# Optimization experiments

Hardware: AMD Instinct MI355X
Metric: run time of the kernel (lower is better)

Reference implementation:

```python
import jax, jax.numpy as jnp
import numpy as np

D_MODEL = 512
LR = 0.01
CLIP = 0.5
B, T = 8, 4096


def setup_inputs() -> dict:
    key = jax.random.key(0)
    k1, k2, k3 = jax.random.split(key, 3)
    x = jax.random.normal(k1, (B, T, D_MODEL), dtype=jnp.float32)
    W_current = jnp.zeros((D_MODEL, D_MODEL), dtype=jnp.float32)
    W_base = jax.random.normal(k2, (D_MODEL, D_MODEL), dtype=jnp.float32) * 0.02
    gate_w = jax.random.normal(k3, (D_MODEL, D_MODEL), dtype=jnp.float32) * (1.0 / np.sqrt(D_MODEL))
    gate_b = jnp.zeros((D_MODEL,), dtype=jnp.float32)
    return {"x": x, "W_current": W_current, "W_base": W_base, "gate_w": gate_w, "gate_b": gate_b}


def reference(x, W_current, W_base, gate_w, gate_b):
    # x: [B, T, D]; W_current, W_base, gate_w: [D, D]; gate_b: [D]
    def step(W_c, x_t):  # x_t: [B, D]
        W = W_base + W_c
        mem_read = x_t @ W.T                       # [B, D]
        gate = jax.nn.sigmoid(x_t @ gate_w.T + gate_b)
        out_t = gate * mem_read
        # fast-weight update (torch.no_grad -> stop_gradient)
        surprise_avg = jax.lax.stop_gradient((x_t - mem_read).mean(axis=0))
        x_avg = jax.lax.stop_gradient(x_t.mean(axis=0))
        dW = jnp.outer(surprise_avg, x_avg)        # [D, D]
        n = jnp.linalg.norm(dW)
        dW = dW * jnp.where(n > CLIP, CLIP / n, 1.0)
        W_new = W_c + LR * dW
        return W_new, out_t

    xs = jnp.swapaxes(x, 0, 1)                     # [T, B, D]
    W_final, outs = jax.lax.scan(step, W_current, xs)
    out = jnp.swapaxes(outs, 0, 1)                 # [B, T, D]
    return out, W_final
```

## Files before the change

kernel.cpp:

```cpp
#include <hip/hip_runtime.h>
#include <math.h>

#define BB 8
#define TT 4096
#define DD 512
constexpr float LRF = 0.01f;

#define OFF_A  0
#define OFF_CU 2097152
#define OFF_G  4194304
#define OFF_P  5242880
#define OFF_BV 5373952
#define OFF_W  5406720
#define OFF_WS 5668864
#define OFF_S  9863168

__global__ void tm_mean(const float* __restrict__ x, float* __restrict__ a) {
    int idx = blockIdx.x * 256 + threadIdx.x;
    float s = 0.f;
#pragma unroll
    for (int b = 0; b < BB; ++b) s += x[b * (TT * DD) + idx];
    a[idx] = s * 0.125f;
}

__global__ void tm_init(const float* __restrict__ wb, const float* __restrict__ wc,
                        float* __restrict__ W, float* __restrict__ Wsnap) {
    int idx = blockIdx.x * 256 + threadIdx.x;
    float v = wb[idx] + wc[idx];
    W[idx] = v;
    Wsnap[idx] = v;
}

__global__ __launch_bounds__(256) void tm_gram(const float* __restrict__ a, float* __restrict__ G) {
    __shared__ float sl[64 * 65];
    __shared__ float tl[64 * 65];
    int bid = blockIdx.x;
    int p = bid >> 4, ts = (bid >> 2) & 3, tt = bid & 3;
    int tid = threadIdx.x;
    int c0 = (tid & 15) * 4, r0 = (tid >> 4) * 4;
    float acc[4][4] = {};
    for (int kt = 0; kt < 8; ++kt) {
        if (kt) __syncthreads();
        for (int l = tid; l < 64 * 16; l += 256) {
            int r = l >> 4, c4 = (l & 15) * 4;
            float4 v = *(const float4*)&a[(p * 256 + ts * 64 + r) * DD + kt * 64 + c4];
            sl[r * 65 + c4] = v.x; sl[r * 65 + c4 + 1] = v.y;
            sl[r * 65 + c4 + 2] = v.z; sl[r * 65 + c4 + 3] = v.w;
            float4 u = *(const float4*)&a[(p * 256 + tt * 64 + r) * DD + kt * 64 + c4];
            tl[r * 65 + c4] = u.x; tl[r * 65 + c4 + 1] = u.y;
            tl[r * 65 + c4 + 2] = u.z; tl[r * 65 + c4 + 3] = u.w;
        }
        __syncthreads();
        for (int kk = 0; kk < 64; ++kk) {
            float as[4], at[4];
#pragma unroll
            for (int q = 0; q < 4; ++q) { as[q] = sl[(r0 + q) * 65 + kk]; at[q] = tl[(c0 + q) * 65 + kk]; }
#pragma unroll
            for (int q = 0; q < 4; ++q)
#pragma unroll
                for (int w2 = 0; w2 < 4; ++w2) acc[q][w2] += as[q] * at[w2];
        }
    }
#pragma unroll
    for (int q = 0; q < 4; ++q) {
        float4 v = make_float4(acc[q][0], acc[q][1], acc[q][2], acc[q][3]);
        *(float4*)&G[p * 65536 + (ts * 64 + r0 + q) * 256 + tt * 64 + c0] = v;
    }
}

__global__ __launch_bounds__(256) void tm_P(const float* __restrict__ a, const float* __restrict__ W,
                                            float* __restrict__ P, int p) {
    __shared__ float al[64 * 65];
    __shared__ float wl[64 * 65];
    int bid = blockIdx.x;
    int bt = bid & 3, bi = bid >> 2;
    int tid = threadIdx.x;
    int c0 = (tid & 15) * 4, r0 = (tid >> 4) * 4;
    float acc[4][4] = {};
    for (int kt = 0; kt < 8; ++kt) {
        if (kt) __syncthreads();
        for (int l = tid; l < 64 * 16; l += 256) {
            int r = l >> 4, c4 = (l & 15) * 4;
            float4 v = *(const float4*)&a[(p * 256 + bt * 64 + r) * DD + kt * 64 + c4];
            al[r * 65 + c4] = v.x; al[r * 65 + c4 + 1] = v.y;
            al[r * 65 + c4 + 2] = v.z; al[r * 65 + c4 + 3] = v.w;
            float4 u = *(const float4*)&W[(bi * 64 + r) * DD + kt * 64 + c4];
            wl[r * 65 + c4] = u.x; wl[r * 65 + c4 + 1] = u.y;
            wl[r * 65 + c4 + 2] = u.z; wl[r * 65 + c4 + 3] = u.w;
        }
        __syncthreads();
        for (int kk = 0; kk < 64; ++kk) {
            float af[4], bf[4];
#pragma unroll
            for (int q = 0; q < 4; ++q) { af[q] = al[(r0 + q) * 65 + kk]; bf[q] = wl[(c0 + q) * 65 + kk]; }
#pragma unroll
            for (int q = 0; q < 4; ++q)
#pragma unroll
                for (int w2 = 0; w2 < 4; ++w2) acc[q][w2] += af[q] * bf[w2];
        }
    }
#pragma unroll
    for (int q = 0; q < 4; ++q) {
        float4 av = *(const float4*)&a[(p * 256 + bt * 64 + r0 + q) * DD + bi * 64 + c0];
        float4 v = make_float4(av.x - acc[q][0], av.y - acc[q][1],
                               av.z - acc[q][2], av.w - acc[q][3]);
        *(float4*)&P[(bt * 64 + r0 + q) * DD + bi * 64 + c0] = v;
    }
}

__global__ __launch_bounds__(256) void tm_corr(const float* __restrict__ P, const float* __restrict__ G,
                                               const float* __restrict__ CU, float* __restrict__ bv,
                                               int p, int j) {
    __shared__ float gsl[64 * 65];
    __shared__ float cul[64 * 65];
    int bd = blockIdx.x;
    int tid = threadIdx.x;
    int c0 = (tid & 15) * 4, r0 = (tid >> 4) * 4;
    const float* Gp = G + p * 65536;
    float acc[4][4] = {};
    for (int kb = 0; kb < j * 64; kb += 64) {
        if (kb) __syncthreads();
        for (int l = tid; l < 64 * 16; l += 256) {
            int r = l >> 4, c4 = (l & 15) * 4;
            float4 v = *(const float4*)&Gp[(kb + r) * 256 + j * 64 + c4];
            gsl[r * 65 + c4] = v.x; gsl[r * 65 + c4 + 1] = v.y;
            gsl[r * 65 + c4 + 2] = v.z; gsl[r * 65 + c4 + 3] = v.w;
            float4 u = *(const float4*)&CU[(p * 256 + kb + r) * DD + bd * 64 + c4];
            cul[r * 65 + c4] = u.x; cul[r * 65 + c4 + 1] = u.y;
            cul[r * 65 + c4 + 2] = u.z; cul[r * 65 + c4 + 3] = u.w;
        }
        __syncthreads();
        for (int kk = 0; kk < 64; ++kk) {
            float gf[4], cf[4];
#pragma unroll
            for (int q = 0; q < 4; ++q) { gf[q] = gsl[kk * 65 + r0 + q]; cf[q] = cul[kk * 65 + c0 + q]; }
#pragma unroll
            for (int q = 0; q < 4; ++q)
#pragma unroll
                for (int w2 = 0; w2 < 4; ++w2) acc[q][w2] += gf[q] * cf[w2];
        }
    }
#pragma unroll
    for (int q = 0; q < 4; ++q) {
        float4 pv = *(const float4*)&P[(j * 64 + r0 + q) * DD + bd * 64 + c0];
        float4 v = make_float4(pv.x - LRF * acc[q][0], pv.y - LRF * acc[q][1],
                               pv.z - LRF * acc[q][2], pv.w - LRF * acc[q][3]);
        *(float4*)&bv[(r0 + q) * DD + bd * 64 + c0] = v;
    }
}

__global__ __launch_bounds__(256) void tm_scan(const float* __restrict__ bv, const float* __restrict__ G,
                                               float* __restrict__ cu, int kchunk) {
    __shared__ float gl[64 * 64];
    __shared__ float part[2][4];
    int tid = threadIdx.x;
    int wid = tid >> 6, lane = tid & 63;
    int p = kchunk >> 2, j = kchunk & 3;
    const float* Gp = G + p * 65536;
    for (int l = tid; l < 64 * 16; l += 256) {
        int r = l >> 4, c4 = (l & 15) * 4;
        float4 v = *(const float4*)&Gp[(j * 64 + r) * 256 + j * 64 + c4];
        *(float4*)&gl[r * 64 + c4] = v;
    }
    float acc0[64], acc1[64];
#pragma unroll
    for (int t = 0; t < 64; ++t) {
        acc0[t] = bv[t * DD + tid];
        acc1[t] = bv[t * DD + tid + 256];
    }
    __syncthreads();
    float* cup = cu + (p * 256 + j * 64) * DD;
#pragma unroll
    for (int s = 0; s < 64; ++s) {
        float u0 = acc0[s], u1 = acc1[s];
        float v = u0 * u0 + u1 * u1;
#pragma unroll
        for (int off = 32; off > 0; off >>= 1) v += __shfl_xor(v, off, 64);
        if (lane == 0) part[s & 1][wid] = v;
        __syncthreads();
        float n2u = part[s & 1][0] + part[s & 1][1] + part[s & 1][2] + part[s & 1][3];
        float n2 = n2u * gl[s * 64 + s];
        float cs = (n2 > 0.25f) ? 0.5f * rsqrtf(n2) : 1.0f;
        cup[s * DD + tid] = cs * u0;
        cup[s * DD + tid + 256] = cs * u1;
        float w0 = (LRF * cs) * u0, w1 = (LRF * cs) * u1;
        int t0 = s + 1;
#pragma unroll
        for (; t0 < 64 && (t0 & 3); ++t0) {
            float g = gl[s * 64 + t0];
            acc0[t0] -= g * w0; acc1[t0] -= g * w1;
        }
#pragma unroll
        for (; t0 < 64; t0 += 4) {
            float4 g4 = *(const float4*)&gl[s * 64 + t0];
            acc0[t0]     -= g4.x * w0; acc1[t0]     -= g4.x * w1;
            acc0[t0 + 1] -= g4.y * w0; acc1[t0 + 1] -= g4.y * w1;
            acc0[t0 + 2] -= g4.z * w0; acc1[t0 + 2] -= g4.z * w1;
            acc0[t0 + 3] -= g4.w * w0; acc1[t0 + 3] -= g4.w * w1;
        }
    }
}

__global__ void tm_wupd(const float* __restrict__ a, const float* __restrict__ cu,
                        float* __restrict__ W, float* __restrict__ Wsnap,
                        const float* __restrict__ wb, float* __restrict__ outW,
                        int p, int snap_p, int is_final) {
    int idx = blockIdx.x * 256 + threadIdx.x;
    int i = idx >> 9, jj = idx & 511;
    const float* cb = cu + p * 256 * DD + i;
    const float* ab = a + p * 256 * DD + jj;
    float s = 0.f;
#pragma unroll 8
    for (int r = 0; r < 256; ++r) s += cb[r * DD] * ab[r * DD];
    float w = W[idx] + LRF * s;
    W[idx] = w;
    if (snap_p >= 0) Wsnap[snap_p * DD * DD + idx] = w;
    if (is_final) outW[idx] = w - wb[idx];
}


__global__ __launch_bounds__(256) void tm_mem(const float* __restrict__ x, const float* __restrict__ Wsnap,
                                              float* __restrict__ out) {
    __shared__ float al[64 * 65];
    __shared__ float bl[64 * 65];
    int bid = blockIdx.x;
    int p = bid >> 8, rem = bid & 255, rt = rem >> 3, it = rem & 7;
    int tid = threadIdx.x;
    int c0 = (tid & 15) * 4, r0 = (tid >> 4) * 4;
    const float* Wp = Wsnap + p * DD * DD;
    float acc[4][4] = {};
    for (int kt = 0; kt < 8; ++kt) {
        if (kt) __syncthreads();
        for (int l = tid; l < 64 * 16; l += 256) {
            int r = l >> 4, c4 = (l & 15) * 4;
            int rloc = rt * 64 + r;
            int grow = ((rloc >> 8) * TT) + p * 256 + (rloc & 255);
            float4 v = *(const float4*)&x[grow * DD + kt * 64 + c4];
            al[r * 65 + c4] = v.x; al[r * 65 + c4 + 1] = v.y;
            al[r * 65 + c4 + 2] = v.z; al[r * 65 + c4 + 3] = v.w;
            float4 u = *(const float4*)&Wp[(it * 64 + r) * DD + kt * 64 + c4];
            bl[r * 65 + c4] = u.x; bl[r * 65 + c4 + 1] = u.y;
            bl[r * 65 + c4 + 2] = u.z; bl[r * 65 + c4 + 3] = u.w;
        }
        __syncthreads();
        for (int kk = 0; kk < 64; ++kk) {
            float af[4], bf[4];
#pragma unroll
            for (int q = 0; q < 4; ++q) { af[q] = al[(r0 + q) * 65 + kk]; bf[q] = bl[(c0 + q) * 65 + kk]; }
#pragma unroll
            for (int q = 0; q < 4; ++q)
#pragma unroll
                for (int w2 = 0; w2 < 4; ++w2) acc[q][w2] += af[q] * bf[w2];
        }
    }
#pragma unroll
    for (int q = 0; q < 4; ++q) {
        int rloc = rt * 64 + r0 + q;
        int grow = ((rloc >> 8) * TT) + p * 256 + (rloc & 255);
        float4 v = make_float4(acc[q][0], acc[q][1], acc[q][2], acc[q][3]);
        *(float4*)&out[grow * DD + it * 64 + c0] = v;
    }
}

__global__ __launch_bounds__(256) void tm_score(const float* __restrict__ x, const float* __restrict__ a,
                                                float* __restrict__ S) {
    __shared__ float al[64 * 65];
    __shared__ float bl[64 * 65];
    int bid = blockIdx.x;
    int st = bid & 3, rt = (bid >> 2) & 31, p = bid >> 7;
    int tid = threadIdx.x;
    int c0 = (tid & 15) * 4, r0 = (tid >> 4) * 4;
    float acc[4][4] = {};
    for (int kt = 0; kt < 8; ++kt) {
        if (kt) __syncthreads();
        for (int l = tid; l < 64 * 16; l += 256) {
            int r = l >> 4, c4 = (l & 15) * 4;
            int rloc = rt * 64 + r;
            int grow = ((rloc >> 8) * TT) + p * 256 + (rloc & 255);
            float4 v = *(const float4*)&x[grow * DD + kt * 64 + c4];
            al[r * 65 + c4] = v.x; al[r * 65 + c4 + 1] = v.y;
            al[r * 65 + c4 + 2] = v.z; al[r * 65 + c4 + 3] = v.w;
            float4 u = *(const float4*)&a[(p * 256 + st * 64 + r) * DD + kt * 64 + c4];
            bl[r * 65 + c4] = u.x; bl[r * 65 + c4 + 1] = u.y;
            bl[r * 65 + c4 + 2] = u.z; bl[r * 65 + c4 + 3] = u.w;
        }
        __syncthreads();
        for (int kk = 0; kk < 64; ++kk) {
            float af[4], bf[4];
#pragma unroll
            for (int q = 0; q < 4; ++q) { af[q] = al[(r0 + q) * 65 + kk]; bf[q] = bl[(c0 + q) * 65 + kk]; }
#pragma unroll
            for (int q = 0; q < 4; ++q)
#pragma unroll
                for (int w2 = 0; w2 < 4; ++w2) acc[q][w2] += af[q] * bf[w2];
        }
    }
#pragma unroll
    for (int q = 0; q < 4; ++q) {
        int rloc = rt * 64 + r0 + q;
        float4 v = make_float4(acc[q][0], acc[q][1], acc[q][2], acc[q][3]);
        *(float4*)&S[(p * 2048 + rloc) * 256 + st * 64 + c0] = v;
    }
}

__global__ __launch_bounds__(256) void tm_apply(const float* __restrict__ S, const float* __restrict__ cu,
                                                float* __restrict__ out) {
    __shared__ float al[64 * 65];
    __shared__ float bl[64 * 65];
    int bid = blockIdx.x;
    int it = bid & 7, rt = (bid >> 3) & 31, p = bid >> 8;
    int tid = threadIdx.x;
    int c0 = (tid & 15) * 4, r0 = (tid >> 4) * 4;
    float acc[4][4] = {};
    for (int kt = 0; kt < 4; ++kt) {
        if (kt) __syncthreads();
        for (int l = tid; l < 64 * 16; l += 256) {
            int r = l >> 4, c4 = (l & 15) * 4;
            int rloc = rt * 64 + r;
            int tq = rloc & 255;
            float4 v = *(const float4*)&S[(p * 2048 + rloc) * 256 + kt * 64 + c4];
            int sb = kt * 64 + c4;
            al[r * 65 + c4]     = (sb + 0 < tq) ? v.x : 0.f;
            al[r * 65 + c4 + 1] = (sb + 1 < tq) ? v.y : 0.f;
            al[r * 65 + c4 + 2] = (sb + 2 < tq) ? v.z : 0.f;
            al[r * 65 + c4 + 3] = (sb + 3 < tq) ? v.w : 0.f;
            float4 u = *(const float4*)&cu[(p * 256 + kt * 64 + r) * DD + it * 64 + c4];
            bl[r * 65 + c4] = u.x; bl[r * 65 + c4 + 1] = u.y;
            bl[r * 65 + c4 + 2] = u.z; bl[r * 65 + c4 + 3] = u.w;
        }
        __syncthreads();
        for (int kk = 0; kk < 64; ++kk) {
            float af[4], bf[4];
#pragma unroll
            for (int q = 0; q < 4; ++q) { af[q] = al[(r0 + q) * 65 + kk]; bf[q] = bl[kk * 65 + c0 + q]; }
#pragma unroll
            for (int q = 0; q < 4; ++q)
#pragma unroll
                for (int w2 = 0; w2 < 4; ++w2) acc[q][w2] += af[q] * bf[w2];
        }
    }
#pragma unroll
    for (int q = 0; q < 4; ++q) {
        int rloc = rt * 64 + r0 + q;
        int grow = ((rloc >> 8) * TT) + p * 256 + (rloc & 255);
        float4 cur = *(float4*)&out[grow * DD + it * 64 + c0];
        cur.x += LRF * acc[q][0]; cur.y += LRF * acc[q][1];
        cur.z += LRF * acc[q][2]; cur.w += LRF * acc[q][3];
        *(float4*)&out[grow * DD + it * 64 + c0] = cur;
    }
}

__global__ __launch_bounds__(256) void tm_gate(const float* __restrict__ x, const float* __restrict__ gw,
                                               const float* __restrict__ gb, float* __restrict__ out) {
    __shared__ float al[64 * 65];
    __shared__ float bl[64 * 65];
    int bid = blockIdx.x;
    int it = bid & 7, rt = bid >> 3;
    int tid = threadIdx.x;
    int c0 = (tid & 15) * 4, r0 = (tid >> 4) * 4;
    float acc[4][4] = {};
    for (int kt = 0; kt < 8; ++kt) {
        if (kt) __syncthreads();
        for (int l = tid; l < 64 * 16; l += 256) {
            int r = l >> 4, c4 = (l & 15) * 4;
            int grow = rt * 64 + r;
            float4 v = *(const float4*)&x[grow * DD + kt * 64 + c4];
            al[r * 65 + c4] = v.x; al[r * 65 + c4 + 1] = v.y;
            al[r * 65 + c4 + 2] = v.z; al[r * 65 + c4 + 3] = v.w;
            float4 u = *(const float4*)&gw[(it * 64 + r) * DD + kt * 64 + c4];
            bl[r * 65 + c4] = u.x; bl[r * 65 + c4 + 1] = u.y;
            bl[r * 65 + c4 + 2] = u.z; bl[r * 65 + c4 + 3] = u.w;
        }
        __syncthreads();
        for (int kk = 0; kk < 64; ++kk) {
            float af[4], bf[4];
#pragma unroll
            for (int q = 0; q < 4; ++q) { af[q] = al[(r0 + q) * 65 + kk]; bf[q] = bl[(c0 + q) * 65 + kk]; }
#pragma unroll
            for (int q = 0; q < 4; ++q)
#pragma unroll
                for (int w2 = 0; w2 < 4; ++w2) acc[q][w2] += af[q] * bf[w2];
        }
    }
#pragma unroll
    for (int q = 0; q < 4; ++q) {
        int grow = rt * 64 + r0 + q;
        float4 cur = *(float4*)&out[grow * DD + it * 64 + c0];
        float z0 = acc[q][0] + gb[it * 64 + c0 + 0];
        float z1 = acc[q][1] + gb[it * 64 + c0 + 1];
        float z2 = acc[q][2] + gb[it * 64 + c0 + 2];
        float z3 = acc[q][3] + gb[it * 64 + c0 + 3];
        cur.x *= 1.f / (1.f + expf(-z0));
        cur.y *= 1.f / (1.f + expf(-z1));
        cur.z *= 1.f / (1.f + expf(-z2));
        cur.w *= 1.f / (1.f + expf(-z3));
        *(float4*)&out[grow * DD + it * 64 + c0] = cur;
    }
}

extern "C" void kernel_launch(void* const* d_in, const int* in_sizes, int n_in,
                              void* d_out, int out_size, void* d_ws, size_t ws_size,
                              hipStream_t stream) {
    const float* x   = (const float*)d_in[0];
    const float* Wc0 = (const float*)d_in[1];
    const float* Wb  = (const float*)d_in[2];
    const float* gw  = (const float*)d_in[3];
    const float* gb  = (const float*)d_in[4];
    float* out  = (float*)d_out;
    float* outW = out + BB * TT * DD;

    float* ws = (float*)d_ws;
    float* A  = ws + OFF_A;
    float* CU = ws + OFF_CU;
    float* G  = ws + OFF_G;
    float* P  = ws + OFF_P;
    float* BV = ws + OFF_BV;
    float* W  = ws + OFF_W;
    float* WS = ws + OFF_WS;
    float* S  = ws + OFF_S;

    tm_mean<<<(TT * DD) / 256, 256, 0, stream>>>(x, A);
    tm_init<<<(DD * DD) / 256, 256, 0, stream>>>(Wb, Wc0, W, WS);
    tm_gram<<<256, 256, 0, stream>>>(A, G);
    tm_P<<<32, 256, 0, stream>>>(A, W, P, 0);

    for (int p = 0; p < 16; ++p) {
        for (int j = 0; j < 4; ++j) {
            tm_corr<<<8, 256, 0, stream>>>(P, G, CU, BV, p, j);
            tm_scan<<<1, 256, 0, stream>>>(BV, G, CU, p * 4 + j);
        }
        if (p < 15) {
            tm_wupd<<<(DD * DD) / 256, 256, 0, stream>>>(A, CU, W, WS, Wb, outW, p, p + 1, 0);
            tm_P<<<32, 256, 0, stream>>>(A, W, P, p + 1);
        }
    }
    tm_wupd<<<(DD * DD) / 256, 256, 0, stream>>>(A, CU, W, WS, Wb, outW, 15, -1, 1);

    tm_mem<<<16 * 256, 256, 0, stream>>>(x, WS, out);
    tm_score<<<16 * 128, 256, 0, stream>>>(x, A, S);
    tm_apply<<<16 * 256, 256, 0, stream>>>(S, CU, out);
    tm_gate<<<512 * 8, 256, 0, stream>>>(x, gw, gb, out);
}
```

Baseline: 8.128 ms.

## Fuse chunk correction and scan into one kernel; transpose GEMM smem tiles

Replaces the per-subchunk tm_corr plus tm_scan pair (8 launches per period) with a single 512-thread tm_sc kernel. It scans all 256 steps of a period with each thread owning one column, applies the forward corrections to later subchunks in registers and global P, and reads the Gram matrix straight from global memory. Separately, the four GEMM kernels now store shared tiles transposed with a stride of 68, which allows float4 LDS reads and packed 2-wide FMAs. This cuts launch overhead on the serial critical path but leaves that path on one workgroup with heavy register use and uncached G reads. It also risks register spills from the b[64] and y[64] arrays.

```diff
diff --git a/kernel.cpp b/kernel.cpp
--- a/kernel.cpp
+++ b/kernel.cpp
@@ -5,6 +5,8 @@
 #define TT 4096
 #define DD 512
 constexpr float LRF = 0.01f;
+
+typedef float v2f __attribute__((ext_vector_type(2)));
 
 #define OFF_A  0
 #define OFF_CU 2097152
@@ -108,95 +110,72 @@
     }
 }
 
-__global__ __launch_bounds__(256) void tm_corr(const float* __restrict__ P, const float* __restrict__ G,
-                                               const float* __restrict__ CU, float* __restrict__ bv,
-                                               int p, int j) {
-    __shared__ float gsl[64 * 65];
-    __shared__ float cul[64 * 65];
-    int bd = blockIdx.x;
-    int tid = threadIdx.x;
-    int c0 = (tid & 15) * 4, r0 = (tid >> 4) * 4;
+__global__ __launch_bounds__(512) void tm_sc(const float* __restrict__ G,
+                                             float* __restrict__ P,
+                                             float* __restrict__ cu, int p) {
+    __shared__ float part[2][8];
+    int tid = threadIdx.x;
+    int wid = tid >> 6, lane = tid & 63;
     const float* Gp = G + p * 65536;
-    float acc[4][4] = {};
-    for (int kb = 0; kb < j * 64; kb += 64) {
-        if (kb) __syncthreads();
-        for (int l = tid; l < 64 * 16; l += 256) {
-            int r = l >> 4, c4 = (l & 15) * 4;
-            float4 v = *(const float4*)&Gp[(kb + r) * 256 + j * 64 + c4];
-            gsl[r * 65 + c4] = v.x; gsl[r * 65 + c4 + 1] = v.y;
-            gsl[r * 65 + c4 + 2] = v.z; gsl[r * 65 + c4 + 3] = v.w;
-            float4 u = *(const float4*)&CU[(p * 256 + kb + r) * DD + bd * 64 + c4];
-            cul[r * 65 + c4] = u.x; cul[r * 65 + c4 + 1] = u.y;
-            cul[r * 65 + c4 + 2] = u.z; cul[r * 65 + c4 + 3] = u.w;
-        }
-        __syncthreads();
-        for (int kk = 0; kk < 64; ++kk) {
-            float gf[4], cf[4];
-#pragma unroll
-            for (int q = 0; q < 4; ++q) { gf[q] = gsl[kk * 65 + r0 + q]; cf[q] = cul[kk * 65 + c0 + q]; }
-#pragma unroll
-            for (int q = 0; q < 4; ++q)
-#pragma unroll
-                for (int w2 = 0; w2 < 4; ++w2) acc[q][w2] += gf[q] * cf[w2];
-        }
-    }
-#pragma unroll
-    for (int q = 0; q < 4; ++q) {
-        float4 pv = *(const float4*)&P[(j * 64 + r0 + q) * DD + bd * 64 + c0];
-        float4 v = make_float4(pv.x - LRF * acc[q][0], pv.y - LRF * acc[q][1],
-                               pv.z - LRF * acc[q][2], pv.w - LRF * acc[q][3]);
-        *(float4*)&bv[(r0 + q) * DD + bd * 64 + c0] = v;
-    }
-}
-
-__global__ __launch_bounds__(256) void tm_scan(const float* __restrict__ bv, const float* __restrict__ G,
-                                               float* __restrict__ cu, int kchunk) {
-    __shared__ float gl[64 * 64];
-    __shared__ float part[2][4];
-    int tid = threadIdx.x;
-    int wid = tid >> 6, lane = tid & 63;
-    int p = kchunk >> 2, j = kchunk & 3;
-    const float* Gp = G + p * 65536;
-    for (int l = tid; l < 64 * 16; l += 256) {
-        int r = l >> 4, c4 = (l & 15) * 4;
-        float4 v = *(const float4*)&Gp[(j * 64 + r) * 256 + j * 64 + c4];
-        *(float4*)&gl[r * 64 + c4] = v;
-    }
-    float acc0[64], acc1[64];
-#pragma unroll
-    for (int t = 0; t < 64; ++t) {
-        acc0[t] = bv[t * DD + tid];
-        acc1[t] = bv[t * DD + tid + 256];
-    }
-    __syncthreads();
-    float* cup = cu + (p * 256 + j * 64) * DD;
-#pragma unroll
-    for (int s = 0; s < 64; ++s) {
-        float u0 = acc0[s], u1 = acc1[s];
-        float v = u0 * u0 + u1 * u1;
-#pragma unroll
-        for (int off = 32; off > 0; off >>= 1) v += __shfl_xor(v, off, 64);
-        if (lane == 0) part[s & 1][wid] = v;
-        __syncthreads();
-        float n2u = part[s & 1][0] + part[s & 1][1] + part[s & 1][2] + part[s & 1][3];
-        float n2 = n2u * gl[s * 64 + s];
-        float cs = (n2 > 0.25f) ? 0.5f * rsqrtf(n2) : 1.0f;
-        cup[s * DD + tid] = cs * u0;
-        cup[s * DD + tid + 256] = cs * u1;
-        float w0 = (LRF * cs) * u0, w1 = (LRF * cs) * u1;
-        int t0 = s + 1;
-#pragma unroll
-        for (; t0 < 64 && (t0 & 3); ++t0) {
-            float g = gl[s * 64 + t0];
-            acc0[t0] -= g * w0; acc1[t0] -= g * w1;
-        }
-#pragma unroll
-        for (; t0 < 64; t0 += 4) {
-            float4 g4 = *(const float4*)&gl[s * 64 + t0];
-            acc0[t0]     -= g4.x * w0; acc1[t0]     -= g4.x * w1;
-            acc0[t0 + 1] -= g4.y * w0; acc1[t0 + 1] -= g4.y * w1;
-            acc0[t0 + 2] -= g4.z * w0; acc1[t0 + 2] -= g4.z * w1;
-            acc0[t0 + 3] -= g4.w * w0; acc1[t0 + 3] -= g4.w * w1;
+    float* cup = cu + p * 256 * DD;
+    float b[64], y[64];
+#pragma unroll
+    for (int t = 0; t < 64; ++t) b[t] = P[t * DD + tid];
+
+    for (int j = 0; j < 4; ++j) {
+        const float* Gj = Gp + (j * 64) * 256;
+#pragma unroll
+        for (int s = 0; s < 64; ++s) {
+            float u = b[s];
+            float v = u * u;
+#pragma unroll
+            for (int off = 32; off > 0; off >>= 1) v += __shfl_xor(v, off, 64);
+            if (lane == 0) part[s & 1][wid] = v;
+            __syncthreads();
+            float n2u = 0.f;
+#pragma unroll
+            for (int w8 = 0; w8 < 8; ++w8) n2u += part[s & 1][w8];
+            float n2 = n2u * Gj[s * 256 + j * 64 + s];
+            float cs = (n2 > 0.25f) ? 0.5f * rsqrtf(n2) : 1.0f;
+            float yv = cs * u;
+            y[s] = yv;
+            float w = LRF * yv;
+            const float* gr = Gj + s * 256 + j * 64;
+#pragma unroll
+            for (int t = s + 1; t < 64; ++t) b[t] -= gr[t] * w;
+        }
+#pragma unroll
+        for (int s2 = 0; s2 < 64; ++s2) cup[(j * 64 + s2) * DD + tid] = y[s2];
+
+        if (j < 3) {
+#pragma unroll
+            for (int t = 0; t < 64; ++t) b[t] = P[((j + 1) * 64 + t) * DD + tid];
+#pragma unroll
+            for (int s = 0; s < 64; ++s) {
+                float w = LRF * y[s];
+                const float* gr = Gj + s * 256 + (j + 1) * 64;
+#pragma unroll
+                for (int t = 0; t < 64; ++t) b[t] -= gr[t] * w;
+            }
+            for (int jf = j + 2; jf < 4; ++jf) {
+                for (int tb = 0; tb < 4; ++tb) {
+                    float acc[16];
+#pragma unroll
+                    for (int t = 0; t < 16; ++t) acc[t] = 0.f;
+#pragma unroll
+                    for (int s = 0; s < 64; ++s) {
+                        const float* gr = Gj + s * 256 + jf * 64 + tb * 16;
+                        float ys = y[s];
+#pragma unroll
+                        for (int t = 0; t < 16; ++t) acc[t] += gr[t] * ys;
+                    }
+#pragma unroll
+                    for (int t = 0; t < 16; ++t) {
+                        int row = (jf * 64 + tb * 16 + t) * DD + tid;
+                        P[row] -= LRF * acc[t];
+                    }
+                }
+            }
         }
     }
 }
@@ -221,175 +200,170 @@
 
 __global__ __launch_bounds__(256) void tm_mem(const float* __restrict__ x, const float* __restrict__ Wsnap,
                                               float* __restrict__ out) {
-    __shared__ float al[64 * 65];
-    __shared__ float bl[64 * 65];
-    int bid = blockIdx.x;
-    int p = bid >> 8, rem = bid & 255, rt = rem >> 3, it = rem & 7;
-    int tid = threadIdx.x;
-    int c0 = (tid & 15) * 4, r0 = (tid >> 4) * 4;
-    const float* Wp = Wsnap + p * DD * DD;
-    float acc[4][4] = {};
+    __shared__ float al[64 * 68];
+    __shared__ float bl[64 * 68];
+    int bid = blockIdx.x;
+    int pp = bid >> 8, rem = bid & 255, rt = rem >> 3, it = rem & 7;
+    int tid = threadIdx.x;
+    int c0 = (tid & 15) * 4, r0 = (tid >> 4) * 4;
+    const float* Wp = Wsnap + pp * DD * DD;
+    v2f acc[4][2] = {};
     for (int kt = 0; kt < 8; ++kt) {
         if (kt) __syncthreads();
         for (int l = tid; l < 64 * 16; l += 256) {
             int r = l >> 4, c4 = (l & 15) * 4;
             int rloc = rt * 64 + r;
-            int grow = ((rloc >> 8) * TT) + p * 256 + (rloc & 255);
+            int grow = ((rloc >> 8) * TT) + pp * 256 + (rloc & 255);
             float4 v = *(const float4*)&x[grow * DD + kt * 64 + c4];
-            al[r * 65 + c4] = v.x; al[r * 65 + c4 + 1] = v.y;
-            al[r * 65 + c4 + 2] = v.z; al[r * 65 + c4 + 3] = v.w;
+            al[(c4 + 0) * 68 + r] = v.x; al[(c4 + 1) * 68 + r] = v.y;
+            al[(c4 + 2) * 68 + r] = v.z; al[(c4 + 3) * 68 + r] = v.w;
             float4 u = *(const float4*)&Wp[(it * 64 + r) * DD + kt * 64 + c4];
-            bl[r * 65 + c4] = u.x; bl[r * 65 + c4 + 1] = u.y;
-            bl[r * 65 + c4 + 2] = u.z; bl[r * 65 + c4 + 3] = u.w;
-        }
-        __syncthreads();
-        for (int kk = 0; kk < 64; ++kk) {
-            float af[4], bf[4];
-#pragma unroll
-            for (int q = 0; q < 4; ++q) { af[q] = al[(r0 + q) * 65 + kk]; bf[q] = bl[(c0 + q) * 65 + kk]; }
-#pragma unroll
-            for (int q = 0; q < 4; ++q)
-#pragma unroll
-                for (int w2 = 0; w2 < 4; ++w2) acc[q][w2] += af[q] * bf[w2];
+            bl[(c4 + 0) * 68 + r] = u.x; bl[(c4 + 1) * 68 + r] = u.y;
+            bl[(c4 + 2) * 68 + r] = u.z; bl[(c4 + 3) * 68 + r] = u.w;
+        }
+        __syncthreads();
+        for (int kk = 0; kk < 64; ++kk) {
+            float4 a4 = *(const float4*)&al[kk * 68 + r0];
+            float4 b4 = *(const float4*)&bl[kk * 68 + c0];
+            v2f blo = {b4.x, b4.y}, bhi = {b4.z, b4.w};
+            float af[4] = {a4.x, a4.y, a4.z, a4.w};
+#pragma unroll
+            for (int q = 0; q < 4; ++q) { acc[q][0] += af[q] * blo; acc[q][1] += af[q] * bhi; }
         }
     }
 #pragma unroll
     for (int q = 0; q < 4; ++q) {
         int rloc = rt * 64 + r0 + q;
-        int grow = ((rloc >> 8) * TT) + p * 256 + (rloc & 255);
-        float4 v = make_float4(acc[q][0], acc[q][1], acc[q][2], acc[q][3]);
+        int grow = ((rloc >> 8) * TT) + pp * 256 + (rloc & 255);
+        float4 v = make_float4(acc[q][0][0], acc[q][0][1], acc[q][1][0], acc[q][1][1]);
         *(float4*)&out[grow * DD + it * 64 + c0] = v;
     }
 }
 
 __global__ __launch_bounds__(256) void tm_score(const float* __restrict__ x, const float* __restrict__ a,
                                                 float* __restrict__ S) {
-    __shared__ float al[64 * 65];
-    __shared__ float bl[64 * 65];
-    int bid = blockIdx.x;
-    int st = bid & 3, rt = (bid >> 2) & 31, p = bid >> 7;
-    int tid = threadIdx.x;
-    int c0 = (tid & 15) * 4, r0 = (tid >> 4) * 4;
-    float acc[4][4] = {};
+    __shared__ float al[64 * 68];
+    __shared__ float bl[64 * 68];
+    int bid = blockIdx.x;
+    int st = bid & 3, rt = (bid >> 2) & 31, pp = bid >> 7;
+    int tid = threadIdx.x;
+    int c0 = (tid & 15) * 4, r0 = (tid >> 4) * 4;
+    v2f acc[4][2] = {};
     for (int kt = 0; kt < 8; ++kt) {
         if (kt) __syncthreads();
         for (int l = tid; l < 64 * 16; l += 256) {
             int r = l >> 4, c4 = (l & 15) * 4;
             int rloc = rt * 64 + r;
-            int grow = ((rloc >> 8) * TT) + p * 256 + (rloc & 255);
+            int grow = ((rloc >> 8) * TT) + pp * 256 + (rloc & 255);
             float4 v = *(const float4*)&x[grow * DD + kt * 64 + c4];
-            al[r * 65 + c4] = v.x; al[r * 65 + c4 + 1] = v.y;
-            al[r * 65 + c4 + 2] = v.z; al[r * 65 + c4 + 3] = v.w;
-            float4 u = *(const float4*)&a[(p * 256 + st * 64 + r) * DD + kt * 64 + c4];
-            bl[r * 65 + c4] = u.x; bl[r * 65 + c4 + 1] = u.y;
-            bl[r * 65 + c4 + 2] = u.z; bl[r * 65 + c4 + 3] = u.w;
-        }
-        __syncthreads();
-        for (int kk = 0; kk < 64; ++kk) {
-            float af[4], bf[4];
-#pragma unroll
-            for (int q = 0; q < 4; ++q) { af[q] = al[(r0 + q) * 65 + kk]; bf[q] = bl[(c0 + q) * 65 + kk]; }
-#pragma unroll
-            for (int q = 0; q < 4; ++q)
-#pragma unroll
-                for (int w2 = 0; w2 < 4; ++w2) acc[q][w2] += af[q] * bf[w2];
+            al[(c4 + 0) * 68 + r] = v.x; al[(c4 + 1) * 68 + r] = v.y;
+            al[(c4 + 2) * 68 + r] = v.z; al[(c4 + 3) * 68 + r] = v.w;
+            float4 u = *(const float4*)&a[(pp * 256 + st * 64 + r) * DD + kt * 64 + c4];
+            bl[(c4 + 0) * 68 + r] = u.x; bl[(c4 + 1) * 68 + r] = u.y;
+            bl[(c4 + 2) * 68 + r] = u.z; bl[(c4 + 3) * 68 + r] = u.w;
+        }
+        __syncthreads();
+        for (int kk = 0; kk < 64; ++kk) {
+            float4 a4 = *(const float4*)&al[kk * 68 + r0];
+            float4 b4 = *(const float4*)&bl[kk * 68 + c0];
+            v2f blo = {b4.x, b4.y}, bhi = {b4.z, b4.w};
+            float af[4] = {a4.x, a4.y, a4.z, a4.w};
+#pragma unroll
+            for (int q = 0; q < 4; ++q) { acc[q][0] += af[q] * blo; acc[q][1] += af[q] * bhi; }
         }
     }
 #pragma unroll
     for (int q = 0; q < 4; ++q) {
         int rloc = rt * 64 + r0 + q;
-        float4 v = make_float4(acc[q][0], acc[q][1], acc[q][2], acc[q][3]);
-        *(float4*)&S[(p * 2048 + rloc) * 256 + st * 64 + c0] = v;
+        float4 v = make_float4(acc[q][0][0], acc[q][0][1], acc[q][1][0], acc[q][1][1]);
+        *(float4*)&S[(pp * 2048 + rloc) * 256 + st * 64 + c0] = v;
     }
 }
 
 __global__ __launch_bounds__(256) void tm_apply(const float* __restrict__ S, const float* __restrict__ cu,
                                                 float* __restrict__ out) {
-    __shared__ float al[64 * 65];
-    __shared__ float bl[64 * 65];
-    int bid = blockIdx.x;
-    int it = bid & 7, rt = (bid >> 3) & 31, p = bid >> 8;
-    int tid = threadIdx.x;
-    int c0 = (tid & 15) * 4, r0 = (tid >> 4) * 4;
-    float acc[4][4] = {};
+    __shared__ float al[64 * 68];
+    __shared__ float bl[64 * 68];
+    int bid = blockIdx.x;
+    int it = bid & 7, rt = (bid >> 3) & 31, pp = bid >> 8;
+    int tid = threadIdx.x;
+    int c0 = (tid & 15) * 4, r0 = (tid >> 4) * 4;
+    v2f acc[4][2] = {};
     for (int kt = 0; kt < 4; ++kt) {
         if (kt) __syncthreads();
         for (int l = tid; l < 64 * 16; l += 256) {
             int r = l >> 4, c4 = (l & 15) * 4;
             int rloc = rt * 64 + r;
             int tq = rloc & 255;
-            float4 v = *(const float4*)&S[(p * 2048 + rloc) * 256 + kt * 64 + c4];
+            float4 v = *(const float4*)&S[(pp * 2048 + rloc) * 256 + kt * 64 + c4];
             int sb = kt * 64 + c4;
-            al[r * 65 + c4]     = (sb + 0 < tq) ? v.x : 0.f;
-            al[r * 65 + c4 + 1] = (sb + 1 < tq) ? v.y : 0.f;
-            al[r * 65 + c4 + 2] = (sb + 2 < tq) ? v.z : 0.f;
-            al[r * 65 + c4 + 3] = (sb + 3 < tq) ? v.w : 0.f;
-            float4 u = *(const float4*)&cu[(p * 256 + kt * 64 + r) * DD + it * 64 + c4];
-            bl[r * 65 + c4] = u.x; bl[r * 65 + c4 + 1] = u.y;
-            bl[r * 65 + c4 + 2] = u.z; bl[r * 65 + c4 + 3] = u.w;
-        }
-        __syncthreads();
-        for (int kk = 0; kk < 64; ++kk) {
-            float af[4], bf[4];
-#pragma unroll
-            for (int q = 0; q < 4; ++q) { af[q] = al[(r0 + q) * 65 + kk]; bf[q] = bl[kk * 65 + c0 + q]; }
-#pragma unroll
-            for (int q = 0; q < 4; ++q)
-#pragma unroll
-                for (int w2 = 0; w2 < 4; ++w2) acc[q][w2] += af[q] * bf[w2];
+            al[(c4 + 0) * 68 + r] = (sb + 0 < tq) ? v.x : 0.f;
+            al[(c4 + 1) * 68 + r] = (sb + 1 < tq) ? v.y : 0.f;
+            al[(c4 + 2) * 68 + r] = (sb + 2 < tq) ? v.z : 0.f;
+            al[(c4 + 3) * 68 + r] = (sb + 3 < tq) ? v.w : 0.f;
+            float4 u = *(const float4*)&cu[(pp * 256 + kt * 64 + r) * DD + it * 64 + c4];
+            *(float4*)&bl[r * 68 + c4] = u;
+        }
+        __syncthreads();
+        for (int kk = 0; kk < 64; ++kk) {
+            float4 a4 = *(const float4*)&al[kk * 68 + r0];
+            float4 b4 = *(const float4*)&bl[kk * 68 + c0];
+            v2f blo = {b4.x, b4.y}, bhi = {b4.z, b4.w};
+            float af[4] = {a4.x, a4.y, a4.z, a4.w};
+#pragma unroll
+            for (int q = 0; q < 4; ++q) { acc[q][0] += af[q] * blo; acc[q][1] += af[q] * bhi; }
         }
     }
 #pragma unroll
     for (int q = 0; q < 4; ++q) {
         int rloc = rt * 64 + r0 + q;
-        int grow = ((rloc >> 8) * TT) + p * 256 + (rloc & 255);
+        int grow = ((rloc >> 8) * TT) + pp * 256 + (rloc & 255);
         float4 cur = *(float4*)&out[grow * DD + it * 64 + c0];
-        cur.x += LRF * acc[q][0]; cur.y += LRF * acc[q][1];
-        cur.z += LRF * acc[q][2]; cur.w += LRF * acc[q][3];
+        cur.x += LRF * acc[q][0][0]; cur.y += LRF * acc[q][0][1];
+        cur.z += LRF * acc[q][1][0]; cur.w += LRF * acc[q][1][1];
         *(float4*)&out[grow * DD + it * 64 + c0] = cur;
     }
 }
 
 __global__ __launch_bounds__(256) void tm_gate(const float* __restrict__ x, const float* __restrict__ gw,
                                                const float* __restrict__ gb, float* __restrict__ out) {
-    __shared__ float al[64 * 65];
-    __shared__ float bl[64 * 65];
+    __shared__ float al[64 * 68];
+    __shared__ float bl[64 * 68];
     int bid = blockIdx.x;
     int it = bid & 7, rt = bid >> 3;
     int tid = threadIdx.x;
     int c0 = (tid & 15) * 4, r0 = (tid >> 4) * 4;
-    float acc[4][4] = {};
+    v2f acc[4][2] = {};
     for (int kt = 0; kt < 8; ++kt) {
         if (kt) __syncthreads();
         for (int l = tid; l < 64 * 16; l += 256) {
             int r = l >> 4, c4 = (l & 15) * 4;
             int grow = rt * 64 + r;
             float4 v = *(const float4*)&x[grow * DD + kt * 64 + c4];
-            al[r * 65 + c4] = v.x; al[r * 65 + c4 + 1] = v.y;
-            al[r * 65 + c4 + 2] = v.z; al[r * 65 + c4 + 3] = v.w;
+            al[(c4 + 0) * 68 + r] = v.x; al[(c4 + 1) * 68 + r] = v.y;
+            al[(c4 + 2) * 68 + r] = v.z; al[(c4 + 3) * 68 + r] = v.w;
             float4 u = *(const float4*)&gw[(it * 64 + r) * DD + kt * 64 + c4];
-            bl[r * 65 + c4] = u.x; bl[r * 65 + c4 + 1] = u.y;
-            bl[r * 65 + c4 + 2] = u.z; bl[r * 65 + c4 + 3] = u.w;
-        }
-        __syncthreads();
-        for (int kk = 0; kk < 64; ++kk) {
-            float af[4], bf[4];
-#pragma unroll
-            for (int q = 0; q < 4; ++q) { af[q] = al[(r0 + q) * 65 + kk]; bf[q] = bl[(c0 + q) * 65 + kk]; }
-#pragma unroll
-            for (int q = 0; q < 4; ++q)
-#pragma unroll
-                for (int w2 = 0; w2 < 4; ++w2) acc[q][w2] += af[q] * bf[w2];
+            bl[(c4 + 0) * 68 + r] = u.x; bl[(c4 + 1) * 68 + r] = u.y;
+            bl[(c4 + 2) * 68 + r] = u.z; bl[(c4 + 3) * 68 + r] = u.w;
+        }
+        __syncthreads();
+        for (int kk = 0; kk < 64; ++kk) {
+            float4 a4 = *(const float4*)&al[kk * 68 + r0];
+            float4 b4 = *(const float4*)&bl[kk * 68 + c0];
+            v2f blo = {b4.x, b4.y}, bhi = {b4.z, b4.w};
+            float af[4] = {a4.x, a4.y, a4.z, a4.w};
+#pragma unroll
+            for (int q = 0; q < 4; ++q) { acc[q][0] += af[q] * blo; acc[q][1] += af[q] * bhi; }
         }
     }
 #pragma unroll
     for (int q = 0; q < 4; ++q) {
         int grow = rt * 64 + r0 + q;
         float4 cur = *(float4*)&out[grow * DD + it * 64 + c0];
-        float z0 = acc[q][0] + gb[it * 64 + c0 + 0];
-        float z1 = acc[q][1] + gb[it * 64 + c0 + 1];
-        float z2 = acc[q][2] + gb[it * 64 + c0 + 2];
-        float z3 = acc[q][3] + gb[it * 64 + c0 + 3];
+        float z0 = acc[q][0][0] + gb[it * 64 + c0 + 0];
+        float z1 = acc[q][0][1] + gb[it * 64 + c0 + 1];
+        float z2 = acc[q][1][0] + gb[it * 64 + c0 + 2];
+        float z3 = acc[q][1][1] + gb[it * 64 + c0 + 3];
         cur.x *= 1.f / (1.f + expf(-z0));
         cur.y *= 1.f / (1.f + expf(-z1));
         cur.z *= 1.f / (1.f + expf(-z2));
@@ -414,7 +388,6 @@
     float* CU = ws + OFF_CU;
     float* G  = ws + OFF_G;
     float* P  = ws + OFF_P;
-    float* BV = ws + OFF_BV;
     float* W  = ws + OFF_W;
     float* WS = ws + OFF_WS;
     float* S  = ws + OFF_S;
@@ -425,10 +398,7 @@
     tm_P<<<32, 256, 0, stream>>>(A, W, P, 0);
 
     for (int p = 0; p < 16; ++p) {
-        for (int j = 0; j < 4; ++j) {
-            tm_corr<<<8, 256, 0, stream>>>(P, G, CU, BV, p, j);
-            tm_scan<<<1, 256, 0, stream>>>(BV, G, CU, p * 4 + j);
-        }
+        tm_sc<<<1, 512, 0, stream>>>(G, P, CU, p);
         if (p < 15) {
             tm_wupd<<<(DD * DD) / 256, 256, 0, stream>>>(A, CU, W, WS, Wb, outW, p, p + 1, 0);
             tm_P<<<32, 256, 0, stream>>>(A, W, P, p + 1);
```

Result: slower. 22.99 ms (+182.9%).
